# Kernel optimization log

Measured on AMD Instinct MI355X. Metric: run time of the kernel, lower is better.

The kernel has to match this reference:

```python
import jax, jax.numpy as jnp
import numpy as np

N_NODES = 10000
N_EDGES = 80000
OBS_DIMS = 128
HIDDEN = 1024
ACT_DIMS = 8
N_GRAPHS = 64


def setup_inputs() -> dict:
    key = jax.random.key(0)
    ks = jax.random.split(key, 8)
    x = jax.random.normal(ks[0], (N_NODES, OBS_DIMS), dtype=jnp.float32)
    edge_index = jax.random.randint(ks[1], (2, N_EDGES), 0, N_NODES, dtype=jnp.int64)
    batch = jnp.sort(jax.random.randint(ks[2], (N_NODES,), 0, N_GRAPHS, dtype=jnp.int64))
    # Glorot-style init for weights, zero bias (as in PyG GCNConv / Linear defaults)
    W1 = jax.random.normal(ks[3], (OBS_DIMS, HIDDEN), dtype=jnp.float32) * (1.0 / np.sqrt(OBS_DIMS))
    b1 = jnp.zeros((HIDDEN,), dtype=jnp.float32)
    W2 = jax.random.normal(ks[4], (HIDDEN, HIDDEN), dtype=jnp.float32) * (1.0 / np.sqrt(HIDDEN))
    b2 = jnp.zeros((HIDDEN,), dtype=jnp.float32)
    Wl = jax.random.normal(ks[5], (HIDDEN, ACT_DIMS), dtype=jnp.float32) * (1.0 / np.sqrt(HIDDEN))
    bl = jnp.zeros((ACT_DIMS,), dtype=jnp.float32)
    return {"x": x, "edge_index": edge_index, "batch": batch,
            "W1": W1, "b1": b1, "W2": W2, "b2": b2, "Wl": Wl, "bl": bl}


def _gcn_conv(x, src, dst, dinv, W, b, n):
    """PyG GCNConv: D^-1/2 (A+I) D^-1/2 X W + b (self-loops already in src/dst)."""
    h = x @ W                                   # [N, out]
    norm = (dinv[src] * dinv[dst])[:, None]      # [E+N, 1]
    msg = h[src] * norm                          # gather + scale
    out = jax.ops.segment_sum(msg, dst, num_segments=n)
    return out + b


def reference(x, edge_index, batch, W1, b1, W2, b2, Wl, bl):
    n = x.shape[0]
    loops = jnp.arange(n, dtype=edge_index.dtype)
    src = jnp.concatenate([edge_index[0], loops])  # add self-loops
    dst = jnp.concatenate([edge_index[1], loops])
    # degree (with self-loops) from destination column, as PyG does
    deg = jax.ops.segment_sum(jnp.ones_like(dst, dtype=x.dtype), dst, num_segments=n)
    dinv = jax.lax.rsqrt(jnp.maximum(deg, 1.0))

    h = jax.nn.relu(_gcn_conv(x, src, dst, dinv, W1, b1, n))
    h = _gcn_conv(h, src, dst, dinv, W2, b2, n)
    h = jnp.tanh(h @ Wl + bl)                    # [N, act_dims]

    # global_mean_pool over batch segment ids
    sums = jax.ops.segment_sum(h, batch, num_segments=N_GRAPHS)
    counts = jax.ops.segment_sum(jnp.ones((n, 1), h.dtype), batch, num_segments=N_GRAPHS)
    return sums / jnp.maximum(counts, 1.0)       # [N_GRAPHS, act_dims]
```

## Files before the change

### kernel.cpp

```cpp
#include <hip/hip_runtime.h>
#include <hip/hip_bf16.h>

#define NNODES 10000
#define NEDGES 80000
#define OBS    128
#define HID    1024
#define ACTD   8
#define NGR    64

typedef __bf16 bf16x8 __attribute__((ext_vector_type(8)));
typedef float  f32x4  __attribute__((ext_vector_type(4)));

__device__ __forceinline__ ushort f2b(float f) {
    union { float f; unsigned int i; } v; v.f = f;
    unsigned int lsb = (v.i >> 16) & 1u;
    unsigned int r = v.i + 0x7fffu + lsb;
    return (ushort)(r >> 16);
}
__device__ __forceinline__ float b2f(ushort u) {
    union { unsigned int i; float f; } v; v.i = ((unsigned int)u) << 16; return v.f;
}
__device__ __forceinline__ int cix(int v, int hi) {
    return v < 0 ? 0 : (v >= hi ? hi - 1 : v);
}

__global__ void k_init(int* degi, float* zacc, float* pool, float* cnt, int n) {
    int i = blockIdx.x * 256 + threadIdx.x;
    if (i < n) degi[i] = 0;
    if (i < n * ACTD) zacc[i] = 0.0f;
    if (i < NGR * ACTD) pool[i] = 0.0f;
    if (i < NGR) cnt[i] = 0.0f;
}

__global__ void k_count(const int* __restrict__ dst, int* degi, int e) {
    int i = blockIdx.x * 256 + threadIdx.x;
    if (i < e) atomicAdd(&degi[cix(dst[i], NNODES)], 1);
}

__global__ __launch_bounds__(1024) void k_scan(const int* __restrict__ degi,
                                               int* rowptr, int* cursor, float* dinv) {
    __shared__ int sums[1024];
    int t = threadIdx.x;
    int base = t * 10;
    int local[10];
    int s = 0;
    #pragma unroll
    for (int k = 0; k < 10; ++k) {
        int i = base + k;
        int v = 0;
        if (i < NNODES) {
            v = degi[i];
            dinv[i] = rsqrtf((float)(v + 1));
        }
        local[k] = s; s += v;
    }
    sums[t] = s;
    __syncthreads();
    int own = s;
    for (int off = 1; off < 1024; off <<= 1) {
        int v = (t >= off) ? sums[t - off] : 0;
        __syncthreads();
        sums[t] += v;
        __syncthreads();
    }
    int excl = sums[t] - own;
    #pragma unroll
    for (int k = 0; k < 10; ++k) {
        int i = base + k;
        if (i < NNODES) { rowptr[i] = excl + local[k]; cursor[i] = excl + local[k]; }
    }
    if (t == 1023) rowptr[NNODES] = sums[1023];
}

__global__ void k_fill(const int* __restrict__ src, const int* __restrict__ dst,
                       const float* __restrict__ dinv, int* cursor,
                       int* __restrict__ esrc, float* __restrict__ coefs, int e) {
    int i = blockIdx.x * 256 + threadIdx.x;
    if (i >= e) return;
    int s = cix(src[i], NNODES), d = cix(dst[i], NNODES);
    int pos = atomicAdd(&cursor[d], 1);
    esrc[pos] = s;
    coefs[pos] = dinv[s] * dinv[d];
}

__global__ __launch_bounds__(256) void k_weights(const float* __restrict__ W1,
                                                 const float* __restrict__ W2,
                                                 const float* __restrict__ Wl,
                                                 const float* __restrict__ b2,
                                                 const float* __restrict__ bl,
                                                 ushort* __restrict__ Wt1,
                                                 ushort* __restrict__ M2bf,
                                                 float* __restrict__ b2l) {
    int blk = blockIdx.x;
    if (blk < 128) {
        __shared__ float tile[32][33];
        int bx = (blk & 31) * 32, by = (blk >> 5) * 32;
        int tx = threadIdx.x & 31, ty = threadIdx.x >> 5;
        #pragma unroll
        for (int i = 0; i < 32; i += 8)
            tile[ty + i][tx] = W1[(size_t)(by + ty + i) * HID + bx + tx];
        __syncthreads();
        #pragma unroll
        for (int i = 0; i < 32; i += 8)
            Wt1[(size_t)(bx + ty + i) * OBS + by + tx] = f2b(tile[tx][ty + i]);
        return;
    }
    int wvid = ((blk - 128) * 256 + (int)threadIdx.x) >> 6;
    int lane = threadIdx.x & 63;
    if (wvid > HID) return;
    const float* row = (wvid == HID) ? b2 : (W2 + (size_t)wvid * HID);
    float acc[ACTD];
    #pragma unroll
    for (int j = 0; j < ACTD; ++j) acc[j] = 0.0f;
    for (int it = 0; it < HID / 64; ++it) {
        int k = it * 64 + lane;
        float w2v = row[k];
        float4 a = *(const float4*)(Wl + (size_t)k * ACTD);
        float4 b = *(const float4*)(Wl + (size_t)k * ACTD + 4);
        acc[0] += w2v * a.x; acc[1] += w2v * a.y; acc[2] += w2v * a.z; acc[3] += w2v * a.w;
        acc[4] += w2v * b.x; acc[5] += w2v * b.y; acc[6] += w2v * b.z; acc[7] += w2v * b.w;
    }
    #pragma unroll
    for (int off = 32; off > 0; off >>= 1)
        #pragma unroll
        for (int j = 0; j < ACTD; ++j)
            acc[j] += __shfl_down(acc[j], off);
    if (lane == 0) {
        if (wvid == HID) {
            #pragma unroll
            for (int j = 0; j < ACTD; ++j) b2l[j] = acc[j] + bl[j];
        } else {
            #pragma unroll
            for (int j = 0; j < ACTD; ++j) M2bf[wvid * ACTD + j] = f2b(acc[j]);
        }
    }
}

__global__ void k_aggx(const float* __restrict__ x, const float* __restrict__ dinv,
                       const int* __restrict__ rowptr, const int* __restrict__ esrc,
                       const float* __restrict__ coefs, ushort* __restrict__ aggbf, int n) {
    int wv = (blockIdx.x * 256 + threadIdx.x) >> 6;
    int lane = threadIdx.x & 63;
    if (wv >= n) return;
    float d = dinv[wv], d2 = d * d;
    float2 xv = *(const float2*)(x + (size_t)wv * OBS + lane * 2);
    float v0 = xv.x * d2, v1 = xv.y * d2;
    int e0 = rowptr[wv], e1 = rowptr[wv + 1];
    for (int e = e0; e < e1; ++e) {
        int s = esrc[e];
        float c = coefs[e];
        float2 sv = *(const float2*)(x + (size_t)s * OBS + lane * 2);
        v0 += sv.x * c; v1 += sv.y * c;
    }
    ushort2 o; o.x = f2b(v0); o.y = f2b(v1);
    *(ushort2*)(aggbf + (size_t)wv * OBS + lane * 2) = o;
}

__global__ __launch_bounds__(256) void k_gemm1_fused(const ushort* __restrict__ A,
                                                     const ushort* __restrict__ Bt,
                                                     const float* __restrict__ bias,
                                                     const ushort* __restrict__ M2bf,
                                                     float* __restrict__ zacc,
                                                     int M) {
    __shared__ ushort buf[128 * 136 + 16 * 128];
    ushort* As    = buf;
    ushort* Bs    = buf + 4096;
    ushort* stage = buf;
    ushort* M2t   = buf + 128 * 136;

    const int t = threadIdx.x;
    const int bm = blockIdx.x, bn = blockIdx.y;
    const int lane = t & 63, wv = t >> 6;
    const int wm = (wv & 1) * 64, wn = (wv >> 1) * 64;
    const int l16 = lane & 15, kg = (lane >> 4) * 8;
    const int r0 = t >> 2;
    const int c0 = (t & 3) << 3;

    if (t < 128) {
        ushort4 a = *(const ushort4*)(M2bf + (size_t)(bn * 128 + t) * ACTD);
        ushort4 b = *(const ushort4*)(M2bf + (size_t)(bn * 128 + t) * ACTD + 4);
        M2t[0 * 128 + t] = a.x; M2t[1 * 128 + t] = a.y;
        M2t[2 * 128 + t] = a.z; M2t[3 * 128 + t] = a.w;
        M2t[4 * 128 + t] = b.x; M2t[5 * 128 + t] = b.y;
        M2t[6 * 128 + t] = b.z; M2t[7 * 128 + t] = b.w;
        #pragma unroll
        for (int j = 8; j < 16; ++j) M2t[j * 128 + t] = 0;
    }

    f32x4 acc[4][4];
    #pragma unroll
    for (int i = 0; i < 4; ++i)
        #pragma unroll
        for (int j = 0; j < 4; ++j)
            acc[i][j] = (f32x4){0.f, 0.f, 0.f, 0.f};

    for (int kt = 0; kt < OBS; kt += 32) {
        if (kt) __syncthreads();
        #pragma unroll
        for (int rd = 0; rd < 2; ++rd) {
            int r = r0 + rd * 64;
            int gr = bm * 128 + r;
            uint4 va = make_uint4(0, 0, 0, 0);
            if (gr < M) va = *(const uint4*)(A + (size_t)gr * OBS + kt + c0);
            *(uint4*)(As + r * 32 + c0) = va;
            int gn = bn * 128 + r;
            uint4 vb = *(const uint4*)(Bt + (size_t)gn * OBS + kt + c0);
            *(uint4*)(Bs + r * 32 + c0) = vb;
        }
        __syncthreads();
        bf16x8 af[4], bfr[4];
        #pragma unroll
        for (int i = 0; i < 4; ++i)
            af[i] = *(const bf16x8*)(As + (wm + i * 16 + l16) * 32 + kg);
        #pragma unroll
        for (int j = 0; j < 4; ++j)
            bfr[j] = *(const bf16x8*)(Bs + (wn + j * 16 + l16) * 32 + kg);
        #pragma unroll
        for (int i = 0; i < 4; ++i)
            #pragma unroll
            for (int j = 0; j < 4; ++j)
                acc[i][j] = __builtin_amdgcn_mfma_f32_16x16x32_bf16(af[i], bfr[j], acc[i][j], 0, 0, 0);
    }
    __syncthreads();

    #pragma unroll
    for (int i = 0; i < 4; ++i) {
        int rowb = wm + i * 16 + (lane >> 4) * 4;
        #pragma unroll
        for (int j = 0; j < 4; ++j) {
            int col = wn + j * 16 + l16;
            float bj = bias[bn * 128 + col];
            #pragma unroll
            for (int r = 0; r < 4; ++r)
                stage[(rowb + r) * 136 + col] = f2b(fmaxf(acc[i][j][r] + bj, 0.0f));
        }
    }
    __syncthreads();

    #pragma unroll
    for (int st = 0; st < 2; ++st) {
        int row0 = wv * 32 + st * 16;
        f32x4 z = (f32x4){0.f, 0.f, 0.f, 0.f};
        #pragma unroll
        for (int kt = 0; kt < 128; kt += 32) {
            bf16x8 a = *(const bf16x8*)(stage + (row0 + l16) * 136 + kt + kg);
            bf16x8 b = *(const bf16x8*)(M2t + l16 * 128 + kt + kg);
            z = __builtin_amdgcn_mfma_f32_16x16x32_bf16(a, b, z, 0, 0, 0);
        }
        if (l16 < ACTD) {
            int rowb = bm * 128 + row0 + (lane >> 4) * 4;
            #pragma unroll
            for (int r = 0; r < 4; ++r)
                if (rowb + r < M)
                    atomicAdd(&zacc[(size_t)(rowb + r) * ACTD + l16], z[r]);
        }
    }
}

__global__ __launch_bounds__(1024) void k_zfinal(const float* __restrict__ zacc,
                                                 const float* __restrict__ dinv,
                                                 const int* __restrict__ rowptr,
                                                 const int* __restrict__ esrc,
                                                 const float* __restrict__ coefs,
                                                 const float* __restrict__ b2l,
                                                 const int* __restrict__ batch,
                                                 float* __restrict__ pool,
                                                 float* __restrict__ cnt, int n) {
    __shared__ float part[NGR * ACTD];
    __shared__ int   partc[NGR];
    int t = threadIdx.x;
    if (t < NGR * ACTD) part[t] = 0.0f;
    if (t < NGR) partc[t] = 0;
    __syncthreads();

    int idx = blockIdx.x * 1024 + t;
    int i = idx >> 3, j = idx & 7;
    if (i < n) {
        float d = dinv[i];
        float v = zacc[idx] * d * d;
        int e0 = rowptr[i], e1 = rowptr[i + 1];
        for (int e = e0; e < e1; ++e)
            v += coefs[e] * zacc[(size_t)esrc[e] * ACTD + j];
        float tz = tanhf(v + b2l[j]);
        int g = cix(batch[i], NGR);
        atomicAdd(&part[g * ACTD + j], tz);
        if (j == 0) atomicAdd(&partc[g], 1);
    }
    __syncthreads();

    int i0 = (blockIdx.x * 1024) >> 3;
    int i1 = (blockIdx.x * 1024 + 1023) >> 3;
    if (i0 >= n) return;
    if (i1 >= n) i1 = n - 1;
    int g0 = cix(batch[i0], NGR), g1 = cix(batch[i1], NGR);
    int ng = g1 - g0 + 1;
    if (t < ng * ACTD)
        atomicAdd(&pool[g0 * ACTD + t], part[g0 * ACTD + t]);
    if (t < ng) {
        int c = partc[g0 + t];
        if (c) atomicAdd(&cnt[g0 + t], (float)c);
    }
}

__global__ void k_final(const float* __restrict__ pool, const float* __restrict__ cnt,
                        float* __restrict__ out, int total) {
    int i = blockIdx.x * 256 + threadIdx.x;
    if (i < total) out[i] = pool[i] / fmaxf(cnt[i >> 3], 1.0f);
}

extern "C" void kernel_launch(void* const* d_in, const int* in_sizes, int n_in,
                              void* d_out, int out_size, void* d_ws, size_t ws_size,
                              hipStream_t stream) {
    const float* x   = (const float*)d_in[0];
    const int*   ei  = (const int*)d_in[1];
    const int*   bat = (const int*)d_in[2];
    const float* W1  = (const float*)d_in[3];
    const float* b1  = (const float*)d_in[4];
    const float* W2  = (const float*)d_in[5];
    const float* b2v = (const float*)d_in[6];
    const float* Wl  = (const float*)d_in[7];
    const float* bl  = (const float*)d_in[8];
    float* out = (float*)d_out;

    const int N = NNODES, E = NEDGES;
    const int* src = ei;
    const int* dst = ei + E;

    char* ws = (char*)d_ws;
    size_t off = 0;
    float*  pool   = (float*)(ws + off); off += 2048;
    float*  cnt    = (float*)(ws + off); off += 256;
    float*  dinv   = (float*)(ws + off); off += 40192;
    int*    degi   = (int*)(ws + off);   off += 40192;
    int*    rowptr = (int*)(ws + off);   off += 40448;
    int*    cursor = (int*)(ws + off);   off += 40192;
    int*    esrc   = (int*)(ws + off);   off += (size_t)E * 4;
    float*  coefs  = (float*)(ws + off); off += (size_t)E * 4;
    float*  b2l    = (float*)(ws + off); off += 256;
    ushort* M2bf   = (ushort*)(ws + off); off += (size_t)HID * ACTD * 2;
    ushort* Wt1    = (ushort*)(ws + off); off += (size_t)HID * OBS * 2;
    float*  zacc   = (float*)(ws + off); off += (size_t)N * ACTD * 4;
    ushort* aggbf  = (ushort*)(ws + off); off += (size_t)N * OBS * 2;

    k_init<<<(N * ACTD + 255) / 256, 256, 0, stream>>>(degi, zacc, pool, cnt, N);
    k_count<<<(E + 255) / 256, 256, 0, stream>>>(dst, degi, E);
    k_scan<<<1, 1024, 0, stream>>>(degi, rowptr, cursor, dinv);
    k_fill<<<(E + 255) / 256, 256, 0, stream>>>(src, dst, dinv, cursor, esrc, coefs, E);

    k_weights<<<128 + ((HID + 1) * 64 + 255) / 256, 256, 0, stream>>>(
        W1, W2, Wl, b2v, bl, Wt1, M2bf, b2l);

    k_aggx<<<(N * 64 + 255) / 256, 256, 0, stream>>>(x, dinv, rowptr, esrc, coefs, aggbf, N);

    k_gemm1_fused<<<dim3((N + 127) / 128, HID / 128), 256, 0, stream>>>(
        aggbf, Wt1, b1, M2bf, zacc, N);

    k_zfinal<<<(N * ACTD + 1023) / 1024, 1024, 0, stream>>>(
        zacc, dinv, rowptr, esrc, coefs, b2l, bat, pool, cnt, N);
    k_final<<<2, 256, 0, stream>>>(pool, cnt, out, NGR * ACTD);
}
```

Measured before the change: 139.1 us.

## Merge init and weight prep kernels, warp-shuffle scan, unroll aggregation, direct-to-LDS GEMM loads

Folds the zero-init kernel into the weight-preparation kernel, which removes one launch. Replaces the shared-memory Hillis-Steele scan with wavefront shuffle scans, so far fewer block barriers are needed. Unrolls the neighbor aggregation loop by two to raise memory-level parallelism. In the first GEMM it switches to 64-wide K tiles loaded with global_load_lds, so data goes straight from global memory to LDS and the number of K iterations and barriers is halved. The risks are LDS layout and bank conflicts from the new 64-wide stride, and the clamped out-of-range rows that are now loaded instead of zero-filled.

```diff
diff --git a/kernel.cpp b/kernel.cpp
--- a/kernel.cpp
+++ b/kernel.cpp
@@ -10,6 +10,8 @@
 
 typedef __bf16 bf16x8 __attribute__((ext_vector_type(8)));
 typedef float  f32x4  __attribute__((ext_vector_type(4)));
+typedef const __attribute__((address_space(1))) unsigned int gl_u32;
+typedef __attribute__((address_space(3))) unsigned int lds_u32;
 
 __device__ __forceinline__ ushort f2b(float f) {
     union { float f; unsigned int i; } v; v.f = f;
@@ -17,19 +19,73 @@
     unsigned int r = v.i + 0x7fffu + lsb;
     return (ushort)(r >> 16);
 }
-__device__ __forceinline__ float b2f(ushort u) {
-    union { unsigned int i; float f; } v; v.i = ((unsigned int)u) << 16; return v.f;
-}
 __device__ __forceinline__ int cix(int v, int hi) {
     return v < 0 ? 0 : (v >= hi ? hi - 1 : v);
 }
 
-__global__ void k_init(int* degi, float* zacc, float* pool, float* cnt, int n) {
-    int i = blockIdx.x * 256 + threadIdx.x;
-    if (i < n) degi[i] = 0;
-    if (i < n * ACTD) zacc[i] = 0.0f;
-    if (i < NGR * ACTD) pool[i] = 0.0f;
-    if (i < NGR) cnt[i] = 0.0f;
+__global__ __launch_bounds__(256) void k_prep(const float* __restrict__ W1,
+                                              const float* __restrict__ W2,
+                                              const float* __restrict__ Wl,
+                                              const float* __restrict__ b2,
+                                              const float* __restrict__ bl,
+                                              ushort* __restrict__ Wt1,
+                                              ushort* __restrict__ M2bf,
+                                              float* __restrict__ b2l,
+                                              float* __restrict__ zacc,
+                                              float* __restrict__ pool,
+                                              float* __restrict__ cnt,
+                                              int* __restrict__ degi) {
+    int blk = blockIdx.x;
+    if (blk >= 385) {
+        int idx = (blk - 385) * 256 + threadIdx.x;
+        if (idx < NNODES * ACTD) zacc[idx] = 0.0f;
+        if (idx < NGR * ACTD) pool[idx] = 0.0f;
+        if (idx < NGR) cnt[idx] = 0.0f;
+        if (idx < NNODES) degi[idx] = 0;
+        return;
+    }
+    if (blk < 128) {
+        __shared__ float tile[32][33];
+        int bx = (blk & 31) * 32, by = (blk >> 5) * 32;
+        int tx = threadIdx.x & 31, ty = threadIdx.x >> 5;
+        #pragma unroll
+        for (int i = 0; i < 32; i += 8)
+            tile[ty + i][tx] = W1[(size_t)(by + ty + i) * HID + bx + tx];
+        __syncthreads();
+        #pragma unroll
+        for (int i = 0; i < 32; i += 8)
+            Wt1[(size_t)(bx + ty + i) * OBS + by + tx] = f2b(tile[tx][ty + i]);
+        return;
+    }
+    int wvid = ((blk - 128) * 256 + (int)threadIdx.x) >> 6;
+    int lane = threadIdx.x & 63;
+    if (wvid > HID) return;
+    const float* row = (wvid == HID) ? b2 : (W2 + (size_t)wvid * HID);
+    float acc[ACTD];
+    #pragma unroll
+    for (int j = 0; j < ACTD; ++j) acc[j] = 0.0f;
+    for (int it = 0; it < HID / 64; ++it) {
+        int k = it * 64 + lane;
+        float w2v = row[k];
+        float4 a = *(const float4*)(Wl + (size_t)k * ACTD);
+        float4 b = *(const float4*)(Wl + (size_t)k * ACTD + 4);
+        acc[0] += w2v * a.x; acc[1] += w2v * a.y; acc[2] += w2v * a.z; acc[3] += w2v * a.w;
+        acc[4] += w2v * b.x; acc[5] += w2v * b.y; acc[6] += w2v * b.z; acc[7] += w2v * b.w;
+    }
+    #pragma unroll
+    for (int off = 32; off > 0; off >>= 1)
+        #pragma unroll
+        for (int j = 0; j < ACTD; ++j)
+            acc[j] += __shfl_down(acc[j], off);
+    if (lane == 0) {
+        if (wvid == HID) {
+            #pragma unroll
+            for (int j = 0; j < ACTD; ++j) b2l[j] = acc[j] + bl[j];
+        } else {
+            #pragma unroll
+            for (int j = 0; j < ACTD; ++j) M2bf[wvid * ACTD + j] = f2b(acc[j]);
+        }
+    }
 }
 
 __global__ void k_count(const int* __restrict__ dst, int* degi, int e) {
@@ -39,8 +95,8 @@
 
 __global__ __launch_bounds__(1024) void k_scan(const int* __restrict__ degi,
                                                int* rowptr, int* cursor, float* dinv) {
-    __shared__ int sums[1024];
-    int t = threadIdx.x;
+    __shared__ int wsum[16];
+    int t = threadIdx.x, lane = t & 63, w = t >> 6;
     int base = t * 10;
     int local[10];
     int s = 0;
@@ -54,22 +110,31 @@
         }
         local[k] = s; s += v;
     }
-    sums[t] = s;
-    __syncthreads();
-    int own = s;
-    for (int off = 1; off < 1024; off <<= 1) {
-        int v = (t >= off) ? sums[t - off] : 0;
-        __syncthreads();
-        sums[t] += v;
-        __syncthreads();
-    }
-    int excl = sums[t] - own;
+    int sc = s;
+    #pragma unroll
+    for (int off = 1; off < 64; off <<= 1) {
+        int u = __shfl_up(sc, off);
+        if (lane >= off) sc += u;
+    }
+    if (lane == 63) wsum[w] = sc;
+    __syncthreads();
+    if (w == 0 && lane < 16) {
+        int v = wsum[lane];
+        #pragma unroll
+        for (int off = 1; off < 16; off <<= 1) {
+            int u = __shfl_up(v, off);
+            if (lane >= off) v += u;
+        }
+        wsum[lane] = v;
+    }
+    __syncthreads();
+    int excl = ((w == 0) ? 0 : wsum[w - 1]) + (sc - s);
     #pragma unroll
     for (int k = 0; k < 10; ++k) {
         int i = base + k;
         if (i < NNODES) { rowptr[i] = excl + local[k]; cursor[i] = excl + local[k]; }
     }
-    if (t == 1023) rowptr[NNODES] = sums[1023];
+    if (t == 0) rowptr[NNODES] = wsum[15];
 }
 
 __global__ void k_fill(const int* __restrict__ src, const int* __restrict__ dst,
@@ -83,59 +148,6 @@
     coefs[pos] = dinv[s] * dinv[d];
 }
 
-__global__ __launch_bounds__(256) void k_weights(const float* __restrict__ W1,
-                                                 const float* __restrict__ W2,
-                                                 const float* __restrict__ Wl,
-                                                 const float* __restrict__ b2,
-                                                 const float* __restrict__ bl,
-                                                 ushort* __restrict__ Wt1,
-                                                 ushort* __restrict__ M2bf,
-                                                 float* __restrict__ b2l) {
-    int blk = blockIdx.x;
-    if (blk < 128) {
-        __shared__ float tile[32][33];
-        int bx = (blk & 31) * 32, by = (blk >> 5) * 32;
-        int tx = threadIdx.x & 31, ty = threadIdx.x >> 5;
-        #pragma unroll
-        for (int i = 0; i < 32; i += 8)
-            tile[ty + i][tx] = W1[(size_t)(by + ty + i) * HID + bx + tx];
-        __syncthreads();
-        #pragma unroll
-        for (int i = 0; i < 32; i += 8)
-            Wt1[(size_t)(bx + ty + i) * OBS + by + tx] = f2b(tile[tx][ty + i]);
-        return;
-    }
-    int wvid = ((blk - 128) * 256 + (int)threadIdx.x) >> 6;
-    int lane = threadIdx.x & 63;
-    if (wvid > HID) return;
-    const float* row = (wvid == HID) ? b2 : (W2 + (size_t)wvid * HID);
-    float acc[ACTD];
-    #pragma unroll
-    for (int j = 0; j < ACTD; ++j) acc[j] = 0.0f;
-    for (int it = 0; it < HID / 64; ++it) {
-        int k = it * 64 + lane;
-        float w2v = row[k];
-        float4 a = *(const float4*)(Wl + (size_t)k * ACTD);
-        float4 b = *(const float4*)(Wl + (size_t)k * ACTD + 4);
-        acc[0] += w2v * a.x; acc[1] += w2v * a.y; acc[2] += w2v * a.z; acc[3] += w2v * a.w;
-        acc[4] += w2v * b.x; acc[5] += w2v * b.y; acc[6] += w2v * b.z; acc[7] += w2v * b.w;
-    }
-    #pragma unroll
-    for (int off = 32; off > 0; off >>= 1)
-        #pragma unroll
-        for (int j = 0; j < ACTD; ++j)
-            acc[j] += __shfl_down(acc[j], off);
-    if (lane == 0) {
-        if (wvid == HID) {
-            #pragma unroll
-            for (int j = 0; j < ACTD; ++j) b2l[j] = acc[j] + bl[j];
-        } else {
-            #pragma unroll
-            for (int j = 0; j < ACTD; ++j) M2bf[wvid * ACTD + j] = f2b(acc[j]);
-        }
-    }
-}
-
 __global__ void k_aggx(const float* __restrict__ x, const float* __restrict__ dinv,
                        const int* __restrict__ rowptr, const int* __restrict__ esrc,
                        const float* __restrict__ coefs, ushort* __restrict__ aggbf, int n) {
@@ -145,12 +157,20 @@
     float d = dinv[wv], d2 = d * d;
     float2 xv = *(const float2*)(x + (size_t)wv * OBS + lane * 2);
     float v0 = xv.x * d2, v1 = xv.y * d2;
-    int e0 = rowptr[wv], e1 = rowptr[wv + 1];
-    for (int e = e0; e < e1; ++e) {
-        int s = esrc[e];
-        float c = coefs[e];
-        float2 sv = *(const float2*)(x + (size_t)s * OBS + lane * 2);
-        v0 += sv.x * c; v1 += sv.y * c;
+    int e = rowptr[wv], e1 = rowptr[wv + 1];
+    for (; e + 2 <= e1; e += 2) {
+        int s0 = esrc[e], s1 = esrc[e + 1];
+        float c0 = coefs[e], c1 = coefs[e + 1];
+        float2 a = *(const float2*)(x + (size_t)s0 * OBS + lane * 2);
+        float2 b = *(const float2*)(x + (size_t)s1 * OBS + lane * 2);
+        v0 += a.x * c0 + b.x * c1;
+        v1 += a.y * c0 + b.y * c1;
+    }
+    if (e < e1) {
+        int s0 = esrc[e];
+        float c0 = coefs[e];
+        float2 a = *(const float2*)(x + (size_t)s0 * OBS + lane * 2);
+        v0 += a.x * c0; v1 += a.y * c0;
     }
     ushort2 o; o.x = f2b(v0); o.y = f2b(v1);
     *(ushort2*)(aggbf + (size_t)wv * OBS + lane * 2) = o;
@@ -164,7 +184,7 @@
                                                      int M) {
     __shared__ ushort buf[128 * 136 + 16 * 128];
     ushort* As    = buf;
-    ushort* Bs    = buf + 4096;
+    ushort* Bs    = buf + 8192;
     ushort* stage = buf;
     ushort* M2t   = buf + 128 * 136;
 
@@ -173,8 +193,6 @@
     const int lane = t & 63, wv = t >> 6;
     const int wm = (wv & 1) * 64, wn = (wv >> 1) * 64;
     const int l16 = lane & 15, kg = (lane >> 4) * 8;
-    const int r0 = t >> 2;
-    const int c0 = (t & 3) << 3;
 
     if (t < 128) {
         ushort4 a = *(const ushort4*)(M2bf + (size_t)(bn * 128 + t) * ACTD);
@@ -194,34 +212,40 @@
         for (int j = 0; j < 4; ++j)
             acc[i][j] = (f32x4){0.f, 0.f, 0.f, 0.f};
 
-    for (int kt = 0; kt < OBS; kt += 32) {
-        if (kt) __syncthreads();
-        #pragma unroll
-        for (int rd = 0; rd < 2; ++rd) {
-            int r = r0 + rd * 64;
-            int gr = bm * 128 + r;
-            uint4 va = make_uint4(0, 0, 0, 0);
-            if (gr < M) va = *(const uint4*)(A + (size_t)gr * OBS + kt + c0);
-            *(uint4*)(As + r * 32 + c0) = va;
+    const int rs = t >> 3;
+    const int cs = (t & 7) * 8;
+    #pragma unroll
+    for (int kt = 0; kt < OBS; kt += 64) {
+        #pragma unroll
+        for (int p = 0; p < 4; ++p) {
+            int r = rs + p * 32;
+            int gr = bm * 128 + r; if (gr >= M) gr = M - 1;
+            __builtin_amdgcn_global_load_lds(
+                (gl_u32*)(A + (size_t)gr * OBS + kt + cs),
+                (lds_u32*)(As + r * 64 + cs), 16, 0, 0);
             int gn = bn * 128 + r;
-            uint4 vb = *(const uint4*)(Bt + (size_t)gn * OBS + kt + c0);
-            *(uint4*)(Bs + r * 32 + c0) = vb;
+            __builtin_amdgcn_global_load_lds(
+                (gl_u32*)(Bt + (size_t)gn * OBS + kt + cs),
+                (lds_u32*)(Bs + r * 64 + cs), 16, 0, 0);
         }
         __syncthreads();
-        bf16x8 af[4], bfr[4];
-        #pragma unroll
-        for (int i = 0; i < 4; ++i)
-            af[i] = *(const bf16x8*)(As + (wm + i * 16 + l16) * 32 + kg);
-        #pragma unroll
-        for (int j = 0; j < 4; ++j)
-            bfr[j] = *(const bf16x8*)(Bs + (wn + j * 16 + l16) * 32 + kg);
-        #pragma unroll
-        for (int i = 0; i < 4; ++i)
+        #pragma unroll
+        for (int k2 = 0; k2 < 64; k2 += 32) {
+            bf16x8 af[4], bfr[4];
+            #pragma unroll
+            for (int i = 0; i < 4; ++i)
+                af[i] = *(const bf16x8*)(As + (wm + i * 16 + l16) * 64 + k2 + kg);
             #pragma unroll
             for (int j = 0; j < 4; ++j)
-                acc[i][j] = __builtin_amdgcn_mfma_f32_16x16x32_bf16(af[i], bfr[j], acc[i][j], 0, 0, 0);
-    }
-    __syncthreads();
+                bfr[j] = *(const bf16x8*)(Bs + (wn + j * 16 + l16) * 64 + k2 + kg);
+            #pragma unroll
+            for (int i = 0; i < 4; ++i)
+                #pragma unroll
+                for (int j = 0; j < 4; ++j)
+                    acc[i][j] = __builtin_amdgcn_mfma_f32_16x16x32_bf16(af[i], bfr[j], acc[i][j], 0, 0, 0);
+        }
+        __syncthreads();
+    }
 
     #pragma unroll
     for (int i = 0; i < 4; ++i) {
@@ -342,14 +366,12 @@
     float*  zacc   = (float*)(ws + off); off += (size_t)N * ACTD * 4;
     ushort* aggbf  = (ushort*)(ws + off); off += (size_t)N * OBS * 2;
 
-    k_init<<<(N * ACTD + 255) / 256, 256, 0, stream>>>(degi, zacc, pool, cnt, N);
+    k_prep<<<698, 256, 0, stream>>>(W1, W2, Wl, b2v, bl, Wt1, M2bf, b2l,
+                                    zacc, pool, cnt, degi);
     k_count<<<(E + 255) / 256, 256, 0, stream>>>(dst, degi, E);
     k_scan<<<1, 1024, 0, stream>>>(degi, rowptr, cursor, dinv);
     k_fill<<<(E + 255) / 256, 256, 0, stream>>>(src, dst, dinv, cursor, esrc, coefs, E);
 
-    k_weights<<<128 + ((HID + 1) * 64 + 255) / 256, 256, 0, stream>>>(
-        W1, W2, Wl, b2v, bl, Wt1, M2bf, b2l);
-
     k_aggx<<<(N * 64 + 255) / 256, 256, 0, stream>>>(x, dinv, rowptr, esrc, coefs, aggbf, N);
 
     k_gemm1_fused<<<dim3((N + 127) / 128, HID / 128), 256, 0, stream>>>(
```

New measurement: 135.5 us. -2.6%, faster.
